# Optimization experiments

Measured on AMD Instinct MI355X. Metric: run time of the kernel, lower is better.

Reference implementation:

```python
import jax, jax.numpy as jnp
import numpy as np

B, S_TXT, S_VID, D, H = 2, 226, 2048, 1024, 16
DH = D // H
LN_EPS = 1e-5


def setup_inputs() -> dict:
    key = jax.random.key(0)
    ks = jax.random.split(key, 10)
    # rotary frequencies, repeated-interleaved for the paired (real, imag) layout
    inv_freq = 1.0 / (10000.0 ** (np.arange(0, DH, 2, dtype=np.float32) / DH))
    angles = np.arange(S_VID, dtype=np.float32)[:, None] * inv_freq[None, :]  # [S_vid, DH/2]
    emb = np.repeat(angles, 2, axis=-1)  # [S_vid, DH]
    w_scale = 0.02
    return {
        "hidden_states": jax.random.normal(ks[0], (B, S_VID, D), jnp.float32),
        "encoder_hidden_states": jax.random.normal(ks[1], (B, S_TXT, D), jnp.float32),
        "cos": jnp.asarray(np.cos(emb)),
        "sin": jnp.asarray(np.sin(emb)),
        "wq": jax.random.normal(ks[2], (D, D), jnp.float32) * w_scale,
        "bq": jnp.zeros((D,), jnp.float32),
        "wk": jax.random.normal(ks[3], (D, D), jnp.float32) * w_scale,
        "bk": jnp.zeros((D,), jnp.float32),
        "wv": jax.random.normal(ks[4], (D, D), jnp.float32) * w_scale,
        "bv": jnp.zeros((D,), jnp.float32),
        "wo": jax.random.normal(ks[5], (D, D), jnp.float32) * w_scale,
        "bo": jnp.zeros((D,), jnp.float32),
        "lnq_w": jnp.ones((DH,), jnp.float32),
        "lnq_b": jnp.zeros((DH,), jnp.float32),
        "lnk_w": jnp.ones((DH,), jnp.float32),
        "lnk_b": jnp.zeros((DH,), jnp.float32),
    }


def _layernorm(x, w, b):
    mu = jnp.mean(x, axis=-1, keepdims=True)
    var = jnp.mean((x - mu) ** 2, axis=-1, keepdims=True)
    return (x - mu) * jax.lax.rsqrt(var + LN_EPS) * w + b


def _apply_rotary(x, cos, sin):
    # x: [B, H, S, DH]; cos/sin: [S, DH]; interleaved (real, imag) pairs (use_real_unbind_dim=-1)
    xp = x.reshape(x.shape[:-1] + (DH // 2, 2))
    x_rot = jnp.stack([-xp[..., 1], xp[..., 0]], axis=-1).reshape(x.shape)
    return x * cos[None, None] + x_rot * sin[None, None]


def reference(hidden_states, encoder_hidden_states, cos, sin, wq, bq, wk, bk, wv, bv,
              wo, bo, lnq_w, lnq_b, lnk_w, lnk_b):
    s_txt = encoder_hidden_states.shape[1]
    h = jnp.concatenate([encoder_hidden_states, hidden_states], axis=1)  # [B, S, D]
    b, s, d = h.shape

    def proj(w, bias):
        return (h @ w.T + bias).reshape(b, s, H, DH).transpose(0, 2, 1, 3)  # [B, H, S, DH]

    q = proj(wq, bq)
    k = proj(wk, bk)
    v = proj(wv, bv)

    q = _layernorm(q, lnq_w, lnq_b)
    k = _layernorm(k, lnk_w, lnk_b)

    # RoPE only on the video (image) tokens
    q = jnp.concatenate([q[:, :, :s_txt], _apply_rotary(q[:, :, s_txt:], cos, sin)], axis=2)
    k = jnp.concatenate([k[:, :, :s_txt], _apply_rotary(k[:, :, s_txt:], cos, sin)], axis=2)

    scale = 1.0 / jnp.sqrt(jnp.asarray(DH, q.dtype))
    scores = jnp.einsum('bhqd,bhkd->bhqk', q, k) * scale
    attn = jax.nn.softmax(scores, axis=-1)
    o = jnp.einsum('bhqk,bhkd->bhqd', attn, v)  # [B, H, S, DH]
    o = o.transpose(0, 2, 1, 3).reshape(b, s, d)
    o = o @ wo.T + bo
    # return (video_hidden_states, text_hidden_states) as in the torch module
    return (o[:, s_txt:], o[:, :s_txt])
```

## Files before the change

### kernel.cpp

```cpp
#include <hip/hip_runtime.h>
#include <hip/hip_bf16.h>

typedef __attribute__((ext_vector_type(4))) float f32x4;
typedef __attribute__((ext_vector_type(16))) float f32x16;
typedef __attribute__((ext_vector_type(8))) short s16x8;
typedef __attribute__((ext_vector_type(4))) short s16x4;

#define GLOAD16(g, s) __builtin_amdgcn_global_load_lds((const __attribute__((address_space(1))) void*)(g), (__attribute__((address_space(3))) void*)(s), 16, 0, 0)

static constexpr int kB    = 2;
static constexpr int kSTXT = 226;
static constexpr int kSVID = 2048;
static constexpr int kD    = 1024;
static constexpr int kS    = kSTXT + kSVID;
static constexpr int kBS   = kB * kS;
static constexpr int kMPAD = 4608;
static constexpr int kSPAD = 2304;
static constexpr int kNT64 = kSPAD / 64;

static __device__ __forceinline__ ushort f2bf(float f) {
  unsigned u = __float_as_uint(f);
  u += 0x7fffu + ((u >> 16) & 1u);
  return (ushort)(u >> 16);
}
static __device__ __forceinline__ float bf2f(short x) {
  return __uint_as_float(((unsigned)(ushort)x) << 16);
}

static __device__ __forceinline__ unsigned cvt_pk_bf16(float lo, float hi) {
  unsigned r;
  asm("v_cvt_pk_bf16_f32 %0, %1, %2" : "=v"(r) : "v"(lo), "v"(hi));
  return r;
}

static __device__ __forceinline__ f32x4 mfma16(s16x8 a, s16x8 b, f32x4 c) {
  return __builtin_amdgcn_mfma_f32_16x16x32_bf16(a, b, c, 0, 0, 0);
}
static __device__ __forceinline__ f32x16 mfma32(s16x8 a, s16x8 b, f32x16 c) {
  return __builtin_amdgcn_mfma_f32_32x32x16_bf16(a, b, c, 0, 0, 0);
}

__global__ __launch_bounds__(256) void k_prep(const float* __restrict__ hid, const float* __restrict__ enc,
    const float* __restrict__ wq, const float* __restrict__ wk,
    const float* __restrict__ wv, const float* __restrict__ wo,
    ushort* __restrict__ Wqkv, ushort* __restrict__ Wo,
    ushort* __restrict__ Xb, ushort* __restrict__ AO,
    ushort* __restrict__ Qb, ushort* __restrict__ Kb, ushort* __restrict__ Vt) {
  int bid = blockIdx.x, tid = threadIdx.x;
  if (bid < 4096) {
    int q = bid * 256 + tid;
    int reg = q >> 18;
    int off = (q & 262143) << 2;
    const float* sp = (reg == 0) ? wq : (reg == 1) ? wk : (reg == 2) ? wv : wo;
    float4 v = *(const float4*)(sp + off);
    ushort4 o;
    o.x = f2bf(v.x); o.y = f2bf(v.y); o.z = f2bf(v.z); o.w = f2bf(v.w);
    ushort* dst = (reg < 3) ? (Wqkv + ((size_t)reg << 20) + off) : (Wo + off);
    *(ushort4*)dst = o;
  } else if (bid < 8764) {
    int q = (bid - 4096) * 256 + tid;
    const int XQ = (kMPAD * kD) / 4;
    if (q < XQ) {
      int row = q >> 8;
      int cq = (q & 255) << 2;
      ushort4 o;
      if (row < kBS) {
        int b = row / kS, s = row - b * kS;
        const float* src = (s < kSTXT) ? (enc + (size_t)(b * kSTXT + s) * kD + cq)
                                       : (hid + (size_t)(b * kSVID + (s - kSTXT)) * kD + cq);
        float4 v = *(const float4*)src;
        o.x = f2bf(v.x); o.y = f2bf(v.y); o.z = f2bf(v.z); o.w = f2bf(v.w);
      } else {
        o.x = 0; o.y = 0; o.z = 0; o.w = 0;
      }
      *(ushort4*)(Xb + (size_t)row * kD + cq) = o;
    } else {
      int p = q - XQ;
      ushort4 z; z.x = 0; z.y = 0; z.z = 0; z.w = 0;
      *(ushort4*)(AO + (size_t)kBS * kD + (size_t)p * 4) = z;
    }
  } else {
    int id = (bid - 8764) * 256 + tid;
    int region = id / 30720;
    int r = id - region * 30720;
    if (region < 2) {
      int bh = r / 960, off = r - bh * 960;
      unsigned* p = (unsigned*)((region == 0 ? Qb : Kb) + (size_t)bh * kSPAD * 64 + (size_t)kS * 64);
      p[off] = 0u;
    } else {
      int row = r / 15, off = r - row * 15;
      unsigned* p = (unsigned*)(Vt + (size_t)row * kSPAD + kS);
      p[off] = 0u;
    }
  }
}

__global__ __launch_bounds__(512) void k_gemmqkv(const ushort* __restrict__ A, const ushort* __restrict__ Bm,
    const float* __restrict__ bq, const float* __restrict__ bk, const float* __restrict__ bv,
    const float* __restrict__ lnqw, const float* __restrict__ lnqb,
    const float* __restrict__ lnkw, const float* __restrict__ lnkb,
    const float* __restrict__ cosb, const float* __restrict__ sinb,
    ushort* __restrict__ Qb, ushort* __restrict__ Kb, ushort* __restrict__ Vt) {
  __shared__ ushort lsA[2][8192];
  __shared__ ushort lsB[2][4096];
  const int K = 1024, nt = 24;
  int bid = blockIdx.x;
  int wg = (bid & 7) * 54 + (bid >> 3);
  int mt = wg / nt, ntl = wg - mt * nt;
  int m0 = mt << 8, n0 = ntl << 7;
  int tid = threadIdx.x;
  int w = tid >> 6, l = tid & 63;
  int wm = (w >> 1) << 6, wn = (w & 1) << 6;
  int lr = l & 15, lh = l >> 4;

  f32x4 acc[4][4] = {};

  int cA0 = tid, cA1 = tid + 512, cB = tid;
  int rA0 = cA0 >> 2, rA1 = cA1 >> 2, rB = cB >> 2;
  int sA0 = ((cA0 & 3) ^ ((cA0 >> 3) & 3)) << 3;
  int sA1 = ((cA1 & 3) ^ ((cA1 >> 3) & 3)) << 3;
  int sB  = ((cB & 3) ^ ((cB >> 3) & 3)) << 3;

#define GISSUE(buf, kk0) do {                                              \
    GLOAD16(A + (size_t)(m0 + rA0) * K + (kk0) + sA0, &lsA[buf][cA0 * 8]); \
    GLOAD16(A + (size_t)(m0 + rA1) * K + (kk0) + sA1, &lsA[buf][cA1 * 8]); \
    GLOAD16(Bm + (size_t)(n0 + rB) * K + (kk0) + sB,  &lsB[buf][cB * 8]);  \
  } while (0)

  GISSUE(0, 0);
  for (int kt = 0; kt < 32; ++kt) {
    int cur = kt & 1;
    __builtin_amdgcn_s_barrier();
    if (kt + 1 < 32) {
      GISSUE(cur ^ 1, (kt + 1) * 32);
      asm volatile("s_waitcnt vmcnt(3)" ::: "memory");
    } else {
      asm volatile("s_waitcnt vmcnt(0)" ::: "memory");
    }
    __builtin_amdgcn_s_barrier();
    __builtin_amdgcn_sched_barrier(0);
    s16x8 af[4], bfr[4];
#pragma unroll
    for (int mi = 0; mi < 4; ++mi) {
      int row = wm + mi * 16 + lr;
      int sl = lh ^ ((row >> 1) & 3);
      af[mi] = *(const s16x8*)&lsA[cur][row * 32 + sl * 8];
    }
#pragma unroll
    for (int ni = 0; ni < 4; ++ni) {
      int row = wn + ni * 16 + lr;
      int sl = lh ^ ((row >> 1) & 3);
      bfr[ni] = *(const s16x8*)&lsB[cur][row * 32 + sl * 8];
    }
    __builtin_amdgcn_s_setprio(1);
#pragma unroll
    for (int mi = 0; mi < 4; ++mi)
#pragma unroll
      for (int ni = 0; ni < 4; ++ni)
        acc[mi][ni] = mfma16(af[mi], bfr[ni], acc[mi][ni]);
    __builtin_amdgcn_s_setprio(0);
  }
#undef GISSUE

  int proj = n0 >> 10;
  int cip0 = (n0 & 1023) + wn;
  int hw = cip0 >> 6;
  const float* bias = (proj == 0) ? bq : (proj == 1) ? bk : bv;
  float bi[4];
#pragma unroll
  for (int ni = 0; ni < 4; ++ni) bi[ni] = bias[cip0 + ni * 16 + lr];

  if (proj < 2) {
    const float* lw = proj ? lnkw : lnqw;
    const float* lb = proj ? lnkb : lnqb;
    const float scale = proj ? 1.0f : 0.125f * 1.4426950408889634f;
    float w4[4], b4[4];
#pragma unroll
    for (int ni = 0; ni < 4; ++ni) { w4[ni] = lw[ni * 16 + lr]; b4[ni] = lb[ni * 16 + lr]; }
    ushort* panel = proj ? Kb : Qb;
#pragma unroll
    for (int mi = 0; mi < 4; ++mi) {
#pragma unroll
      for (int r = 0; r < 4; ++r) {
        int grow = m0 + wm + mi * 16 + lh * 4 + r;
        float v0 = acc[mi][0][r] + bi[0], v1 = acc[mi][1][r] + bi[1];
        float v2 = acc[mi][2][r] + bi[2], v3 = acc[mi][3][r] + bi[3];
        float sum = (v0 + v1) + (v2 + v3);
        sum += __shfl_xor(sum, 1); sum += __shfl_xor(sum, 2);
        sum += __shfl_xor(sum, 4); sum += __shfl_xor(sum, 8);
        float mu = sum * (1.0f / 64.0f);
        float d0 = v0 - mu, d1 = v1 - mu, d2 = v2 - mu, d3 = v3 - mu;
        float ss = (d0 * d0 + d1 * d1) + (d2 * d2 + d3 * d3);
        ss += __shfl_xor(ss, 1); ss += __shfl_xor(ss, 2);
        ss += __shfl_xor(ss, 4); ss += __shfl_xor(ss, 8);
        float rstd = rsqrtf(ss * (1.0f / 64.0f) + 1e-5f);
        float n0v = d0 * rstd * w4[0] + b4[0];
        float n1v = d1 * rstd * w4[1] + b4[1];
        float n2v = d2 * rstd * w4[2] + b4[2];
        float n3v = d3 * rstd * w4[3] + b4[3];
        int bb = grow >= kS;
        int s = grow - (bb ? kS : 0);
        bool valid = (grow < kBS) && (s < kS);
        if (valid) {
          if (s >= kSTXT) {
            int pos = s - kSTXT;
            const float* cr = cosb + (size_t)pos * 64;
            const float* sr = sinb + (size_t)pos * 64;
            float sg = (lr & 1) ? 1.0f : -1.0f;
            float p0 = __shfl_xor(n0v, 1), p1 = __shfl_xor(n1v, 1);
            float p2 = __shfl_xor(n2v, 1), p3 = __shfl_xor(n3v, 1);
            n0v = n0v * cr[lr]      + sg * p0 * sr[lr];
            n1v = n1v * cr[16 + lr] + sg * p1 * sr[16 + lr];
            n2v = n2v * cr[32 + lr] + sg * p2 * sr[32 + lr];
            n3v = n3v * cr[48 + lr] + sg * p3 * sr[48 + lr];
          }
          ushort* pr = panel + (size_t)((bb << 4) + hw) * kSPAD * 64 + (size_t)s * 64;
          pr[lr]      = f2bf(n0v * scale);
          pr[16 + lr] = f2bf(n1v * scale);
          pr[32 + lr] = f2bf(n2v * scale);
          pr[48 + lr] = f2bf(n3v * scale);
        }
      }
    }
  } else {
    bool fast = (m0 != 2048) && (m0 != 4352);
#pragma unroll
    for (int mi = 0; mi < 4; ++mi) {
      int grow0 = m0 + wm + mi * 16 + lh * 4;
#pragma unroll
      for (int ni = 0; ni < 4; ++ni) {
        int d = ni * 16 + lr;
        float f0 = acc[mi][ni][0] + bi[ni], f1 = acc[mi][ni][1] + bi[ni];
        float f2 = acc[mi][ni][2] + bi[ni], f3 = acc[mi][ni][3] + bi[ni];
        if (fast) {
          int bb = grow0 >= kS;
          int s0 = grow0 - (bb ? kS : 0);
          unsigned* pr = (unsigned*)(Vt + (size_t)((bb << 4) + hw) * 64 * kSPAD + (size_t)d * kSPAD + s0);
          pr[0] = cvt_pk_bf16(f0, f1);
          pr[1] = cvt_pk_bf16(f2, f3);
        } else {
          float fv[4] = {f0, f1, f2, f3};
#pragma unroll
          for (int j = 0; j < 4; ++j) {
            int grow = grow0 + j;
            int bb = grow >= kS;
            int s = grow - (bb ? kS : 0);
            if (grow < kBS && s < kS)
              Vt[(size_t)((bb << 4) + hw) * 64 * kSPAD + (size_t)d * kSPAD + s] = f2bf(fv[j]);
          }
        }
      }
    }
  }
}

__global__ __launch_bounds__(256) void k_gemmo(const ushort* __restrict__ A, const ushort* __restrict__ Bm,
                                               float* __restrict__ OutF, const float* __restrict__ bias) {
  __shared__ ushort lsA[2][4096];
  __shared__ ushort lsB[2][4096];
  const int K = 1024, nt = 8;
  int mt = blockIdx.x / nt, ntl = blockIdx.x - mt * nt;
  int m0 = mt << 7, n0 = ntl << 7;
  int tid = threadIdx.x;
  int w = tid >> 6, l = tid & 63;
  int wm = (w >> 1) << 6, wn = (w & 1) << 6;
  int lr = l & 15, lh = l >> 4;

  f32x4 acc[4][4] = {};

  int c0 = w * 64 + l, c1 = c0 + 256;
  int dA0 = (w * 64) << 3, dA1 = (256 + w * 64) << 3;

#define GISSUE(buf, kk0) do {                                                       \
    GLOAD16(A + (size_t)(m0 + (c0 >> 2)) * K + (kk0) + ((c0 & 3) << 3), &lsA[buf][dA0]); \
    GLOAD16(A + (size_t)(m0 + (c1 >> 2)) * K + (kk0) + ((c1 & 3) << 3), &lsA[buf][dA1]); \
    GLOAD16(Bm + (size_t)(n0 + (c0 >> 2)) * K + (kk0) + ((c0 & 3) << 3), &lsB[buf][dA0]); \
    GLOAD16(Bm + (size_t)(n0 + (c1 >> 2)) * K + (kk0) + ((c1 & 3) << 3), &lsB[buf][dA1]); \
  } while (0)

  GISSUE(0, 0);
  for (int kt = 0; kt < 32; ++kt) {
    int cur = kt & 1;
    __builtin_amdgcn_s_barrier();
    if (kt + 1 < 32) {
      GISSUE(cur ^ 1, (kt + 1) * 32);
      asm volatile("s_waitcnt vmcnt(4)" ::: "memory");
    } else {
      asm volatile("s_waitcnt vmcnt(0)" ::: "memory");
    }
    __builtin_amdgcn_s_barrier();
    __builtin_amdgcn_sched_barrier(0);
    s16x8 af[4], bfr[4];
#pragma unroll
    for (int mi = 0; mi < 4; ++mi) af[mi] = *(const s16x8*)&lsA[cur][(wm + mi * 16 + lr) * 32 + lh * 8];
#pragma unroll
    for (int ni = 0; ni < 4; ++ni) bfr[ni] = *(const s16x8*)&lsB[cur][(wn + ni * 16 + lr) * 32 + lh * 8];
    __builtin_amdgcn_s_setprio(1);
#pragma unroll
    for (int mi = 0; mi < 4; ++mi)
#pragma unroll
      for (int ni = 0; ni < 4; ++ni)
        acc[mi][ni] = mfma16(af[mi], bfr[ni], acc[mi][ni]);
    __builtin_amdgcn_s_setprio(0);
  }
#undef GISSUE

#pragma unroll
  for (int mi = 0; mi < 4; ++mi) {
#pragma unroll
    for (int ni = 0; ni < 4; ++ni) {
#pragma unroll
      for (int r = 0; r < 4; ++r) {
        int row = m0 + wm + mi * 16 + lh * 4 + r;
        int col = n0 + wn + ni * 16 + lr;
        if (row < kBS) {
          float v = acc[mi][ni][r] + bias[col];
          int b = row / kS, s = row - b * kS;
          size_t o = (s >= kSTXT) ? ((size_t)(b * kSVID + s - kSTXT) * kD + col)
                                  : ((size_t)kB * kSVID * kD + (size_t)(b * kSTXT + s) * kD + col);
          OutF[o] = v;
        }
      }
    }
  }
}

__global__ __launch_bounds__(256, 4) void k_attn(const ushort* __restrict__ Q, const ushort* __restrict__ K,
                                                 const ushort* __restrict__ Vt,
                                                 ushort* __restrict__ Opb, float* __restrict__ Ml) {
  __shared__ ushort lsK[2][4096];
  __shared__ ushort lsVt[2][4096];

  int bid = blockIdx.x;
  int wg = (bid & 7) * 216 + (bid >> 3);
  int bq = wg / 3, sp = wg - bq * 3;
  int bh = bq / 18, qb = bq - bh * 18;
  const ushort* Qp = Q + (size_t)bh * kSPAD * 64;
  const char* Kg = (const char*)(K + (size_t)bh * kSPAD * 64);
  const char* Vg = (const char*)(Vt + (size_t)bh * 64 * kSPAD);

  int tid = threadIdx.x, w = tid >> 6, l = tid & 63;
  int lq = l & 31, h = l >> 5;
  int q0 = qb * 128 + w * 32;

  s16x8 aq[4];
#pragma unroll
  for (int sl = 0; sl < 4; ++sl)
    aq[sl] = *(const s16x8*)(Qp + (size_t)(q0 + lq) * 64 + sl * 16 + h * 8);

  f32x16 o0 = {}, o1 = {};
  float lsum = 0.0f;

  int ksrc[2], vsrc[2], kdst[2];
#pragma unroll
  for (int i = 0; i < 2; ++i) {
    int c = tid + 256 * i;
    kdst[i] = c * 16;
    ksrc[i] = (c * 16) ^ (((c >> 3) & 7) << 4);
    int vr = c >> 3;
    vsrc[i] = vr * (kSPAD * 2) + (((c & 7) * 16) ^ ((vr & 7) << 4));
  }

#define ISSUE_TILE(buf, t) do {                                             \
    GLOAD16(Kg + (size_t)(t) * 8192 + ksrc[0], (char*)lsK[buf] + kdst[0]);  \
    GLOAD16(Kg + (size_t)(t) * 8192 + ksrc[1], (char*)lsK[buf] + kdst[1]);  \
    GLOAD16(Vg + (size_t)(t) * 128 + vsrc[0],  (char*)lsVt[buf] + kdst[0]); \
    GLOAD16(Vg + (size_t)(t) * 128 + vsrc[1],  (char*)lsVt[buf] + kdst[1]); \
  } while (0)

  int t0 = sp * 12;
  ISSUE_TILE(0, t0);

  int swz = (lq & 7) << 4;
  for (int tt = 0; tt < 12; ++tt) {
    int t = t0 + tt;
    int cur = tt & 1;
    __builtin_amdgcn_s_barrier();
    if (tt + 1 < 12) {
      ISSUE_TILE(cur ^ 1, t + 1);
      asm volatile("s_waitcnt vmcnt(4)" ::: "memory");
    } else {
      asm volatile("s_waitcnt vmcnt(0)" ::: "memory");
    }
    __builtin_amdgcn_s_barrier();
    __builtin_amdgcn_sched_barrier(0);

    f32x16 s0 = {}, s1 = {};
    __builtin_amdgcn_s_setprio(1);
#pragma unroll
    for (int sl = 0; sl < 4; ++sl) {
      int cb = h * 16 + sl * 32;
      s16x8 kf0 = *(const s16x8*)((const char*)lsK[cur] + ((lq * 128 + cb) ^ swz));
      s16x8 kf1 = *(const s16x8*)((const char*)lsK[cur] + (((lq + 32) * 128 + cb) ^ swz));
      s0 = mfma32(kf0, aq[sl], s0);
      s1 = mfma32(kf1, aq[sl], s1);
    }
    __builtin_amdgcn_s_setprio(0);

    if (t == kNT64 - 1) {
      int kv0 = t * 64;
#pragma unroll
      for (int reg = 0; reg < 16; ++reg) {
        int kl = (reg & 3) + 8 * (reg >> 2) + 4 * h;
        if (kv0 + kl >= kS) s0[reg] = -1e30f;
        if (kv0 + 32 + kl >= kS) s1[reg] = -1e30f;
      }
    }

    float ls0 = 0.0f, ls1 = 0.0f;
#pragma unroll
    for (int i = 0; i < 16; ++i) { s0[i] = exp2f(s0[i]); ls0 += s0[i]; }
#pragma unroll
    for (int i = 0; i < 16; ++i) { s1[i] = exp2f(s1[i]); ls1 += s1[i]; }
    lsum += ls0 + ls1;

    __builtin_amdgcn_s_setprio(1);
#pragma unroll
    for (int ks2 = 0; ks2 < 4; ++ks2) {
      unsigned A0, A1, B0, B1;
      if (ks2 == 0) {
        A0 = cvt_pk_bf16(s0[0], s0[1]);  A1 = cvt_pk_bf16(s0[2], s0[3]);
        B0 = cvt_pk_bf16(s0[4], s0[5]);  B1 = cvt_pk_bf16(s0[6], s0[7]);
      } else if (ks2 == 1) {
        A0 = cvt_pk_bf16(s0[8], s0[9]);  A1 = cvt_pk_bf16(s0[10], s0[11]);
        B0 = cvt_pk_bf16(s0[12], s0[13]); B1 = cvt_pk_bf16(s0[14], s0[15]);
      } else if (ks2 == 2) {
        A0 = cvt_pk_bf16(s1[0], s1[1]);  A1 = cvt_pk_bf16(s1[2], s1[3]);
        B0 = cvt_pk_bf16(s1[4], s1[5]);  B1 = cvt_pk_bf16(s1[6], s1[7]);
      } else {
        A0 = cvt_pk_bf16(s1[8], s1[9]);  A1 = cvt_pk_bf16(s1[10], s1[11]);
        B0 = cvt_pk_bf16(s1[12], s1[13]); B1 = cvt_pk_bf16(s1[14], s1[15]);
      }
      asm volatile("v_permlane32_swap_b32 %0, %1" : "+v"(A0), "+v"(B0));
      asm volatile("v_permlane32_swap_b32 %0, %1" : "+v"(A1), "+v"(B1));
      union { unsigned u[4]; s16x8 v; } pu;
      pu.u[0] = A0; pu.u[1] = A1; pu.u[2] = B0; pu.u[3] = B1;
      int cb = h * 16 + ks2 * 32;
      s16x8 vf0 = *(const s16x8*)((const char*)lsVt[cur] + ((lq * 128 + cb) ^ swz));
      s16x8 vf1 = *(const s16x8*)((const char*)lsVt[cur] + (((lq + 32) * 128 + cb) ^ swz));
      o0 = mfma32(vf0, pu.v, o0);
      o1 = mfma32(vf1, pu.v, o1);
    }
    __builtin_amdgcn_s_setprio(0);
  }
#undef ISSUE_TILE

  lsum += __shfl_xor(lsum, 32);

  ushort* op = Opb + ((size_t)(sp * 576 + bq) << 13);
  int qrow = w * 32 + lq;
#pragma unroll
  for (int g = 0; g < 4; ++g) {
    int d0 = 8 * g + 4 * h;
    uint2 pk;
    pk.x = cvt_pk_bf16(o0[4 * g], o0[4 * g + 1]);
    pk.y = cvt_pk_bf16(o0[4 * g + 2], o0[4 * g + 3]);
    *(uint2*)&op[qrow * 64 + d0] = pk;
    pk.x = cvt_pk_bf16(o1[4 * g], o1[4 * g + 1]);
    pk.y = cvt_pk_bf16(o1[4 * g + 2], o1[4 * g + 3]);
    *(uint2*)&op[qrow * 64 + 32 + d0] = pk;
  }
  float* ml = Ml + ((size_t)(sp * 576 + bq) << 7);
  if (h == 0) ml[qrow] = lsum;
}

__global__ __launch_bounds__(256) void k_combine(const ushort* __restrict__ Opb, const float* __restrict__ Ml,
                                                 ushort* __restrict__ AO) {
  int bq = blockIdx.x;
  int bh = bq / 18, q128 = bq - bh * 18;
  int b = bh >> 4, hd = bh & 15;
  int tid = threadIdx.x;
#pragma unroll
  for (int i = 0; i < 8; ++i) {
    int eid = i * 256 + tid;
    int q = eid >> 4;
    int d4 = (eid & 15) << 2;
    int srow = q128 * 128 + q;
    if (srow >= kS) continue;
    float den = 0.0f, e0 = 0.0f, e1 = 0.0f, e2 = 0.0f, e3 = 0.0f;
#pragma unroll
    for (int s = 0; s < 3; ++s) {
      den += Ml[((size_t)(s * 576 + bq) << 7) + q];
      uint2 pk = *(const uint2*)(Opb + ((size_t)(s * 576 + bq) << 13) + (q << 6) + d4);
      e0 += bf2f((short)(pk.x & 0xffffu));
      e1 += bf2f((short)(pk.x >> 16));
      e2 += bf2f((short)(pk.y & 0xffffu));
      e3 += bf2f((short)(pk.y >> 16));
    }
    float inv = 1.0f / den;
    uint2 opk;
    opk.x = (unsigned)f2bf(e0 * inv) | ((unsigned)f2bf(e1 * inv) << 16);
    opk.y = (unsigned)f2bf(e2 * inv) | ((unsigned)f2bf(e3 * inv) << 16);
    *(uint2*)&AO[(size_t)(b * kS + srow) * kD + hd * 64 + d4] = opk;
  }
}

extern "C" void kernel_launch(void* const* d_in, const int* in_sizes, int n_in,
                              void* d_out, int out_size, void* d_ws, size_t ws_size,
                              hipStream_t stream) {
  const float* hid  = (const float*)d_in[0];
  const float* enc  = (const float*)d_in[1];
  const float* cosb = (const float*)d_in[2];
  const float* sinb = (const float*)d_in[3];
  const float* wq   = (const float*)d_in[4];
  const float* bq   = (const float*)d_in[5];
  const float* wk   = (const float*)d_in[6];
  const float* bk   = (const float*)d_in[7];
  const float* wv   = (const float*)d_in[8];
  const float* bv   = (const float*)d_in[9];
  const float* wo   = (const float*)d_in[10];
  const float* bo   = (const float*)d_in[11];
  const float* lnqw = (const float*)d_in[12];
  const float* lnqb = (const float*)d_in[13];
  const float* lnkw = (const float*)d_in[14];
  const float* lnkb = (const float*)d_in[15];

  if (ws_size < 112197632u) return;

  char* ws = (char*)d_ws;
  ushort* Xb   = (ushort*)(ws);
  ushort* Wqkv = (ushort*)(ws + 9437184);
  ushort* Wo   = (ushort*)(ws + 15728640);
  ushort* Vtb  = (ushort*)(ws + 17825792);
  ushort* Opb  = (ushort*)(ws + 27262976);
  float*  Ml   = (float*)(ws + 55574528);
  ushort* Qb   = (ushort*)(ws + 74448896);
  ushort* Kb   = (ushort*)(ws + 83886080);
  ushort* AO   = (ushort*)(ws + 102760448);

  float* out = (float*)d_out;

  k_prep<<<dim3(9124), dim3(256), 0, stream>>>(hid, enc, wq, wk, wv, wo,
      Wqkv, Wo, Xb, AO, Qb, Kb, Vtb);
  k_gemmqkv<<<dim3(432), dim3(512), 0, stream>>>(Xb, Wqkv, bq, bk, bv,
      lnqw, lnqb, lnkw, lnkb, cosb, sinb, Qb, Kb, Vtb);
  k_attn<<<dim3(1728), dim3(256), 0, stream>>>(Qb, Kb, Vtb, Opb, Ml);
  k_combine<<<dim3(576), dim3(256), 0, stream>>>(Opb, Ml, AO);
  k_gemmo<<<dim3(36 * 8), dim3(256), 0, stream>>>(AO, Wo, out, bo);
}
```

Measured before the change: 168.6 us.

## Swizzle output-GEMM LDS, use raw exp2, compute softmax row sums via MFMA

Three changes. The output-projection GEMM now writes and reads its LDS tiles with an XOR swizzle on the 16-byte column slot, aiming to remove LDS bank conflicts on fragment reads. The attention kernel replaces exp2f with the hardware v_exp_f32 builtin. It also drops the scalar row-sum accumulation in favour of an extra MFMA that multiplies a ones vector by the bf16 probabilities. That moves the reductions onto the matrix unit at the cost of one more MFMA per k-step and rounding the sums to bf16 precision.

```diff
diff --git a/kernel.cpp b/kernel.cpp
--- a/kernel.cpp
+++ b/kernel.cpp
@@ -31,6 +31,14 @@
   unsigned r;
   asm("v_cvt_pk_bf16_f32 %0, %1, %2" : "=v"(r) : "v"(lo), "v"(hi));
   return r;
+}
+
+static __device__ __forceinline__ float fexp2(float x) {
+#if __has_builtin(__builtin_amdgcn_exp2f)
+  return __builtin_amdgcn_exp2f(x);
+#else
+  float r; asm("v_exp_f32 %0, %1" : "=v"(r) : "v"(x)); return r;
+#endif
 }
 
 static __device__ __forceinline__ f32x4 mfma16(s16x8 a, s16x8 b, f32x4 c) {
@@ -269,13 +277,15 @@
   f32x4 acc[4][4] = {};
 
   int c0 = w * 64 + l, c1 = c0 + 256;
-  int dA0 = (w * 64) << 3, dA1 = (256 + w * 64) << 3;
-
-#define GISSUE(buf, kk0) do {                                                       \
-    GLOAD16(A + (size_t)(m0 + (c0 >> 2)) * K + (kk0) + ((c0 & 3) << 3), &lsA[buf][dA0]); \
-    GLOAD16(A + (size_t)(m0 + (c1 >> 2)) * K + (kk0) + ((c1 & 3) << 3), &lsA[buf][dA1]); \
-    GLOAD16(Bm + (size_t)(n0 + (c0 >> 2)) * K + (kk0) + ((c0 & 3) << 3), &lsB[buf][dA0]); \
-    GLOAD16(Bm + (size_t)(n0 + (c1 >> 2)) * K + (kk0) + ((c1 & 3) << 3), &lsB[buf][dA1]); \
+  int r0 = c0 >> 2, r1 = c1 >> 2;
+  int s0o = ((c0 & 3) ^ ((c0 >> 3) & 3)) << 3;
+  int s1o = ((c1 & 3) ^ ((c1 >> 3) & 3)) << 3;
+
+#define GISSUE(buf, kk0) do {                                              \
+    GLOAD16(A + (size_t)(m0 + r0) * K + (kk0) + s0o, &lsA[buf][c0 * 8]);   \
+    GLOAD16(A + (size_t)(m0 + r1) * K + (kk0) + s1o, &lsA[buf][c1 * 8]);   \
+    GLOAD16(Bm + (size_t)(n0 + r0) * K + (kk0) + s0o, &lsB[buf][c0 * 8]);  \
+    GLOAD16(Bm + (size_t)(n0 + r1) * K + (kk0) + s1o, &lsB[buf][c1 * 8]);  \
   } while (0)
 
   GISSUE(0, 0);
@@ -292,9 +302,17 @@
     __builtin_amdgcn_sched_barrier(0);
     s16x8 af[4], bfr[4];
 #pragma unroll
-    for (int mi = 0; mi < 4; ++mi) af[mi] = *(const s16x8*)&lsA[cur][(wm + mi * 16 + lr) * 32 + lh * 8];
-#pragma unroll
-    for (int ni = 0; ni < 4; ++ni) bfr[ni] = *(const s16x8*)&lsB[cur][(wn + ni * 16 + lr) * 32 + lh * 8];
+    for (int mi = 0; mi < 4; ++mi) {
+      int row = wm + mi * 16 + lr;
+      int sl = lh ^ ((row >> 1) & 3);
+      af[mi] = *(const s16x8*)&lsA[cur][row * 32 + sl * 8];
+    }
+#pragma unroll
+    for (int ni = 0; ni < 4; ++ni) {
+      int row = wn + ni * 16 + lr;
+      int sl = lh ^ ((row >> 1) & 3);
+      bfr[ni] = *(const s16x8*)&lsB[cur][row * 32 + sl * 8];
+    }
     __builtin_amdgcn_s_setprio(1);
 #pragma unroll
     for (int mi = 0; mi < 4; ++mi)
@@ -348,8 +366,11 @@
   for (int sl = 0; sl < 4; ++sl)
     aq[sl] = *(const s16x8*)(Qp + (size_t)(q0 + lq) * 64 + sl * 16 + h * 8);
 
-  f32x16 o0 = {}, o1 = {};
-  float lsum = 0.0f;
+  s16x8 ones;
+#pragma unroll
+  for (int j = 0; j < 8; ++j) ones[j] = (short)0x3F80;
+
+  f32x16 o0 = {}, o1 = {}, oL = {};
 
   int ksrc[2], vsrc[2], kdst[2];
 #pragma unroll
@@ -407,12 +428,10 @@
       }
     }
 
-    float ls0 = 0.0f, ls1 = 0.0f;
-#pragma unroll
-    for (int i = 0; i < 16; ++i) { s0[i] = exp2f(s0[i]); ls0 += s0[i]; }
-#pragma unroll
-    for (int i = 0; i < 16; ++i) { s1[i] = exp2f(s1[i]); ls1 += s1[i]; }
-    lsum += ls0 + ls1;
+#pragma unroll
+    for (int i = 0; i < 16; ++i) s0[i] = fexp2(s0[i]);
+#pragma unroll
+    for (int i = 0; i < 16; ++i) s1[i] = fexp2(s1[i]);
 
     __builtin_amdgcn_s_setprio(1);
 #pragma unroll
@@ -440,12 +459,13 @@
       s16x8 vf1 = *(const s16x8*)((const char*)lsVt[cur] + (((lq + 32) * 128 + cb) ^ swz));
       o0 = mfma32(vf0, pu.v, o0);
       o1 = mfma32(vf1, pu.v, o1);
+      oL = mfma32(ones, pu.v, oL);
     }
     __builtin_amdgcn_s_setprio(0);
   }
 #undef ISSUE_TILE
 
-  lsum += __shfl_xor(lsum, 32);
+  float lsum = oL[0];
 
   ushort* op = Opb + ((size_t)(sp * 576 + bq) << 13);
   int qrow = w * 32 + lq;
```

After: 156.9 us (median of 2 runs). 1.07x faster.
